# Kernel tuning notes

Hardware: AMD Instinct MI355X
Metric: run time of the kernel (lower is better)

Reference implementation:

```python
import jax, jax.numpy as jnp
import numpy as np

N = 50000          # num nodes
E = 800000         # num edges
DIN = 128          # in_channels
C = 64             # out_channels per head
H = 2              # heads
ED = 32            # edge_dim


def setup_inputs() -> dict:
    key = jax.random.key(0)
    ks = jax.random.split(key, 12)
    s = 1.0 / np.sqrt(DIN)
    se = 1.0 / np.sqrt(ED)
    return {
        "x": jax.random.normal(ks[0], (N, DIN), dtype=jnp.float32),
        "edge_index": jax.random.randint(ks[1], (2, E), 0, N, dtype=jnp.int32),
        "edge_attr": jax.random.normal(ks[2], (E, ED), dtype=jnp.float32),
        "Wq": jax.random.uniform(ks[3], (DIN, H * C), jnp.float32, -s, s),
        "bq": jax.random.uniform(ks[4], (H * C,), jnp.float32, -s, s),
        "Wk": jax.random.uniform(ks[5], (DIN, H * C), jnp.float32, -s, s),
        "bk": jax.random.uniform(ks[6], (H * C,), jnp.float32, -s, s),
        "Wv": jax.random.uniform(ks[7], (DIN, H * C), jnp.float32, -s, s),
        "bv": jax.random.uniform(ks[8], (H * C,), jnp.float32, -s, s),
        "We": jax.random.uniform(ks[9], (ED, H * C), jnp.float32, -se, se),
        "Wskip": jax.random.uniform(ks[10], (DIN, H * C), jnp.float32, -s, s),
        "bskip": jax.random.uniform(ks[11], (H * C,), jnp.float32, -s, s),
    }


def reference(x, edge_index, edge_attr, Wq, bq, Wk, bk, Wv, bv, We, Wskip, bskip):
    src, dst = edge_index[0], edge_index[1]
    # node-level projections [N, H, C]
    q = (x @ Wq + bq).reshape(N, H, C)
    k = (x @ Wk + bk).reshape(N, H, C)
    v = (x @ Wv + bv).reshape(N, H, C)
    e = (edge_attr @ We).reshape(E, H, C)  # lin_edge, no bias

    # per-edge gather
    q_e = q[dst]              # [E, H, C]
    k_e = k[src] + e          # key gets edge features
    alpha = jnp.einsum("ehc,ehc->eh", q_e, k_e) / jnp.sqrt(jnp.float32(C))

    # segment softmax over incoming edges of each dst node
    m = jax.ops.segment_max(alpha, dst, num_segments=N)       # [N, H]
    alpha = jnp.exp(alpha - m[dst])
    denom = jax.ops.segment_sum(alpha, dst, num_segments=N)   # [N, H]
    alpha = alpha / (denom[dst] + 1e-16)

    # weighted aggregation of values (value also gets edge features)
    msg = (v[src] + e) * alpha[..., None]                     # [E, H, C]
    out = jax.ops.segment_sum(msg, dst, num_segments=N)       # [N, H, C]
    out = out.reshape(N, H * C)

    # root weight skip connection (concat=True, beta=False)
    return out + x @ Wskip + bskip
```

## Files before the change

kernel.cpp:

```cpp
#include <hip/hip_runtime.h>
#include <cstdint>

#define NN 50000
#define EE 800000
#define DINC 128
#define HC 128
#define EDC 32
#define CAP 56
#define TILES 1563
#define GEMM_BLKS 6252
#define SCAT_BLKS 3125
#define NB_SCAN 196

typedef __attribute__((ext_vector_type(8))) short short8;
typedef __attribute__((ext_vector_type(4))) float floatx4;

__device__ __forceinline__ unsigned int pk2(float a, float b){
  unsigned int ua = __float_as_uint(a), ub = __float_as_uint(b);
  ua = (ua + 0x7FFFu + ((ua >> 16) & 1u)) >> 16;
  ub = (ub + 0x7FFFu + ((ub >> 16) & 1u)) & 0xFFFF0000u;
  return ua | ub;
}
__device__ __forceinline__ float bflo(unsigned int p){ return __uint_as_float(p << 16); }
__device__ __forceinline__ float bfhi(unsigned int p){ return __uint_as_float(p & 0xFFFF0000u); }

__global__ __launch_bounds__(256) void k_prew(
    const float* __restrict__ Wq, const float* __restrict__ Wk,
    const float* __restrict__ Wv, const float* __restrict__ Wsk,
    unsigned int* __restrict__ Wp)
{
  int idx = blockIdx.x*256 + threadIdx.x;
  int mat = idx >> 13;
  int r   = idx & 8191;
  int kp  = r >> 7;
  int n   = r & 127;
  const float* W = (mat==0)?Wq:(mat==1)?Wk:(mat==2)?Wv:Wsk;
  Wp[(mat<<13) + n*64 + kp] = pk2(W[(2*kp)*HC + n], W[(2*kp+1)*HC + n]);
}

__global__ __launch_bounds__(256) void k_fused(
    const float* __restrict__ x, const unsigned int* __restrict__ Wp,
    const float* __restrict__ bq, const float* __restrict__ bk,
    const float* __restrict__ bv, const float* __restrict__ bsk,
    const int* __restrict__ ei,
    unsigned int* __restrict__ qbf, unsigned int* __restrict__ kvb,
    float* __restrict__ out, int* __restrict__ cnt, int* __restrict__ eidl,
    const int do_scatter)
{
  __shared__ unsigned int smem[32*132];

  if (do_scatter && blockIdx.x >= GEMM_BLKS){
    int e = (blockIdx.x - GEMM_BLKS)*256 + threadIdx.x;
    if (e < EE){
      int d = ei[EE + e];
      int pos = atomicAdd(cnt + d, 1);
      if (pos < CAP) eidl[d*CAP + pos] = e;
    }
    return;
  }

  unsigned int* sx = smem;
  float* facc = (float*)smem;

  const int tid = threadIdx.x;
  const int mat = blockIdx.x & 3;
  const int bm  = (blockIdx.x >> 2) * 32;
  const float* bi = (mat==0)?bq:(mat==1)?bk:(mat==2)?bv:bsk;
  const unsigned int* wp = Wp + (mat<<13);

  for (int idx = tid; idx < 32*32; idx += 256){
    int row = idx >> 5, kq = idx & 31;
    int gr = bm + row;
    unsigned int p0 = 0u, p1 = 0u;
    if (gr < NN){
      float4 v = *(const float4*)(x + (size_t)gr*DINC + 4*kq);
      p0 = pk2(v.x, v.y); p1 = pk2(v.z, v.w);
    }
    sx[row*68 + 2*kq]     = p0;
    sx[row*68 + 2*kq + 1] = p1;
  }
  __syncthreads();

  const int l = tid & 63, wid = tid >> 6;
  const int lm = l & 15, ks = l >> 4;
  const int n0 = wid * 32;

  floatx4 acc[2][2];
  #pragma unroll
  for (int mt=0;mt<2;mt++)
    #pragma unroll
    for (int nt=0;nt<2;nt++) acc[mt][nt] = (floatx4){0.f,0.f,0.f,0.f};

  #pragma unroll
  for (int kb = 0; kb < 4; ++kb){
    short8 a0 = *(const short8*)(sx + lm*68        + kb*16 + ks*4);
    short8 a1 = *(const short8*)(sx + (16+lm)*68   + kb*16 + ks*4);
    short8 b0 = *(const short8*)(wp + (n0+lm)*64    + kb*16 + ks*4);
    short8 b1 = *(const short8*)(wp + (n0+16+lm)*64 + kb*16 + ks*4);
    acc[0][0] = __builtin_amdgcn_mfma_f32_16x16x32_bf16(a0, b0, acc[0][0], 0, 0, 0);
    acc[0][1] = __builtin_amdgcn_mfma_f32_16x16x32_bf16(a0, b1, acc[0][1], 0, 0, 0);
    acc[1][0] = __builtin_amdgcn_mfma_f32_16x16x32_bf16(a1, b0, acc[1][0], 0, 0, 0);
    acc[1][1] = __builtin_amdgcn_mfma_f32_16x16x32_bf16(a1, b1, acc[1][1], 0, 0, 0);
  }
  __syncthreads();

  #pragma unroll
  for (int mt=0;mt<2;mt++)
    #pragma unroll
    for (int nt=0;nt<2;nt++)
      #pragma unroll
      for (int r=0;r<4;r++){
        int row = mt*16 + ks*4 + r;
        int col = n0 + nt*16 + lm;
        facc[row*132 + col] = acc[mt][nt][r];
      }
  __syncthreads();

  for (int idx = tid; idx < 32*64; idx += 256){
    int row = idx >> 6, cp = idx & 63;
    int gr = bm + row;
    if (gr >= NN) continue;
    float2 vv = *(const float2*)(facc + row*132 + 2*cp);
    float2 bb = *(const float2*)(bi + 2*cp);
    float v0 = vv.x + bb.x, v1 = vv.y + bb.y;
    if (mat == 0)      qbf[gr*64 + cp] = pk2(v0, v1);
    else if (mat == 1) kvb[(size_t)gr*128 + cp]      = pk2(v0, v1);
    else if (mat == 2) kvb[(size_t)gr*128 + 64 + cp] = pk2(v0, v1);
    else *(float2*)(out + (size_t)gr*HC + 2*cp) = make_float2(v0, v1);
  }
}

__global__ __launch_bounds__(256) void k_count(const int* __restrict__ ei,
    int* __restrict__ cnt)
{
  int e = blockIdx.x*256 + threadIdx.x;
  if (e < EE) atomicAdd(cnt + ei[EE + e], 1);
}
__global__ __launch_bounds__(256) void k_blksum(const int* __restrict__ cnt,
    int* __restrict__ bsum)
{
  __shared__ int s[256];
  int t = threadIdx.x, i = blockIdx.x*256 + t;
  s[t] = (i < NN) ? cnt[i] : 0;
  __syncthreads();
  for (int d = 128; d > 0; d >>= 1){
    if (t < d) s[t] += s[t + d];
    __syncthreads();
  }
  if (t == 0) bsum[blockIdx.x] = s[0];
}
__global__ __launch_bounds__(256) void k_bscan(const int* __restrict__ bsum,
    int* __restrict__ bpre)
{
  __shared__ int s[256];
  int t = threadIdx.x;
  int v = (t < NB_SCAN) ? bsum[t] : 0;
  s[t] = v;
  __syncthreads();
  for (int d = 1; d < 256; d <<= 1){
    int u = (t >= d) ? s[t - d] : 0;
    __syncthreads();
    s[t] += u;
    __syncthreads();
  }
  if (t < NB_SCAN) bpre[t] = s[t] - v;
}
__global__ __launch_bounds__(256) void k_scan3(const int* __restrict__ cnt,
    const int* __restrict__ bpre, int* __restrict__ off, int* __restrict__ woff)
{
  __shared__ int s[256];
  int t = threadIdx.x, i = blockIdx.x*256 + t;
  int v = (i < NN) ? cnt[i] : 0;
  s[t] = v;
  __syncthreads();
  for (int d = 1; d < 256; d <<= 1){
    int u = (t >= d) ? s[t - d] : 0;
    __syncthreads();
    s[t] += u;
    __syncthreads();
  }
  if (i < NN){
    int o = bpre[blockIdx.x] + s[t] - v;
    off[i] = o; woff[i] = o;
  }
}
__global__ __launch_bounds__(256) void k_scatter(const int* __restrict__ ei,
    int* __restrict__ woff, int* __restrict__ eidl)
{
  int e = blockIdx.x*256 + threadIdx.x;
  if (e < EE){
    int d = ei[EE + e];
    int pos = atomicAdd(woff + d, 1);
    eidl[pos] = e;
  }
}

__global__ __launch_bounds__(256) void k_agg(
    const float* __restrict__ eattr, const float* __restrict__ We,
    const unsigned int* __restrict__ qbf, const unsigned int* __restrict__ kvb,
    const int* __restrict__ ei,
    const int* __restrict__ cnt, const int* __restrict__ off,
    const int* __restrict__ eidl, const int fixed,
    float* __restrict__ out)
{
  __shared__ float sWeT[128*33];
  const int tid = threadIdx.x;
  for (int idx = tid; idx < EDC*HC; idx += 256){
    int jj = idx >> 7, col = idx & 127;
    sWeT[col*33 + jj] = We[idx];
  }
  __syncthreads();

  const int wid = tid >> 6, l = tid & 63;
  const int node = blockIdx.x*4 + wid;
  const int h = l >> 5, j = l & 31;

  int deg = cnt[node]; if (deg > CAP) deg = CAP;
  const size_t beg = fixed ? (size_t)node*CAP : (size_t)off[node];
  int eidL = 0, srcL = 0;
  if (deg > 0){
    eidL = eidl[beg + ((l < deg) ? l : 0)];
    srcL = ei[eidL];
  }

  unsigned int qp = qbf[node*64 + l];
  float q0 = bflo(qp), q1 = bfhi(qp);
  float Pl = 0.f;
  {
    const unsigned int* qrow = qbf + node*64 + h*32;
    const float* wt = sWeT + (h*64)*33 + j;
    #pragma unroll 8
    for (int cc = 0; cc < 32; ++cc){
      unsigned int up = qrow[cc];
      Pl += bflo(up)*wt[(2*cc)*33] + bfhi(up)*wt[(2*cc+1)*33];
    }
  }

  float acc0=0.f, acc1=0.f, wea=0.f, den=0.f;
  if (deg > 0){
    float eav[4]; unsigned int kk[4], vv[4];
    #pragma unroll
    for (int t = 0; t < 4; ++t){
      int it  = (t < deg) ? t : 0;
      int eid = __shfl(eidL, it, 64);
      int src = __shfl(srcL, it, 64);
      eav[t] = eattr[(size_t)eid*EDC + j];
      kk[t]  = kvb[(size_t)src*128 + l];
      vv[t]  = kvb[(size_t)src*128 + 64 + l];
    }
    for (int i = 0; i < deg; i += 4){
      float eavn[4]; unsigned int kkn[4], vvn[4];
      const int inext = i + 4;
      if (inext < deg){
        #pragma unroll
        for (int t = 0; t < 4; ++t){
          int it  = (inext + t < deg) ? inext + t : inext;
          int eid = __shfl(eidL, it, 64);
          int src = __shfl(srcL, it, 64);
          eavn[t] = eattr[(size_t)eid*EDC + j];
          kkn[t]  = kvb[(size_t)src*128 + l];
          vvn[t]  = kvb[(size_t)src*128 + 64 + l];
        }
      }
      float p[4];
      #pragma unroll
      for (int t = 0; t < 4; ++t)
        p[t] = q0*bflo(kk[t]) + q1*bfhi(kk[t]) + Pl*eav[t];
      #pragma unroll
      for (int s = 1; s < 32; s <<= 1){
        #pragma unroll
        for (int t = 0; t < 4; ++t) p[t] += __shfl_xor(p[t], s, 32);
      }
      const int nb = deg - i;
      #pragma unroll
      for (int t = 0; t < 4; ++t){
        float a = __expf(p[t] * 0.125f);
        if (t > 0) a = (t < nb) ? a : 0.f;
        den  += a;
        acc0 += a*bflo(vv[t]);
        acc1 += a*bfhi(vv[t]);
        wea  += a*eav[t];
      }
      #pragma unroll
      for (int t = 0; t < 4; ++t){ eav[t] = eavn[t]; kk[t] = kkn[t]; vv[t] = vvn[t]; }
    }
  }

  float rden = 1.0f/(den + 1e-16f);
  float e0 = 0.f, e1 = 0.f;
  const float* w0 = sWeT + (2*l)*33;
  const float* w1 = sWeT + (2*l+1)*33;
  #pragma unroll 8
  for (int jj = 0; jj < 32; ++jj){
    float w = __shfl(wea, h*32 + jj, 64);
    e0 += w*w0[jj]; e1 += w*w1[jj];
  }
  float2 sk = *(const float2*)(out + (size_t)node*HC + 2*l);
  float2 o;
  o.x = sk.x + (acc0 + e0)*rden;
  o.y = sk.y + (acc1 + e1)*rden;
  *(float2*)(out + (size_t)node*HC + 2*l) = o;
}

extern "C" void kernel_launch(void* const* d_in, const int* in_sizes, int n_in,
                              void* d_out, int out_size, void* d_ws, size_t ws_size,
                              hipStream_t stream)
{
  const float* x   = (const float*)d_in[0];
  const int*   ei  = (const int*)d_in[1];
  const float* ea  = (const float*)d_in[2];
  const float* Wq  = (const float*)d_in[3];
  const float* bq  = (const float*)d_in[4];
  const float* Wk  = (const float*)d_in[5];
  const float* bk  = (const float*)d_in[6];
  const float* Wv  = (const float*)d_in[7];
  const float* bv  = (const float*)d_in[8];
  const float* We  = (const float*)d_in[9];
  const float* Wsk = (const float*)d_in[10];
  const float* bsk = (const float*)d_in[11];
  float* out = (float*)d_out;

  char* ws = (char*)d_ws;
  unsigned int* qbf = (unsigned int*)(ws);
  unsigned int* kvb = (unsigned int*)(ws + 12800000);
  int* cnt = (int*)(ws + 38400000);

  hipMemsetAsync(cnt, 0, NN*sizeof(int), stream);

  if (ws_size >= 50000000ull){
    int* eidl = (int*)(ws + 38600000);
    unsigned int* Wp = (unsigned int*)(ws + 49800064);
    k_prew<<<128, 256, 0, stream>>>(Wq, Wk, Wv, Wsk, Wp);
    k_fused<<<GEMM_BLKS + SCAT_BLKS, 256, 0, stream>>>(
        x, Wp, bq, bk, bv, bsk, ei, qbf, kvb, out, cnt, eidl, 1);
    k_agg<<<12500, 256, 0, stream>>>(ea, We, qbf, kvb, ei,
                                     cnt, (const int*)nullptr, eidl, 1, out);
  } else {
    int* off  = (int*)(ws + 38600000);
    int* woff = (int*)(ws + 38800000);
    int* bsum = (int*)(ws + 39000000);
    int* bpre = (int*)(ws + 39001024);
    int* eidl = (int*)(ws + 39002048);
    unsigned int* Wp = (unsigned int*)(ws + 42202112);
    k_prew<<<128, 256, 0, stream>>>(Wq, Wk, Wv, Wsk, Wp);
    k_fused<<<GEMM_BLKS, 256, 0, stream>>>(
        x, Wp, bq, bk, bv, bsk, ei, qbf, kvb, out, cnt, nullptr, 0);
    k_count  <<<SCAT_BLKS, 256, 0, stream>>>(ei, cnt);
    k_blksum <<<NB_SCAN, 256, 0, stream>>>(cnt, bsum);
    k_bscan  <<<1, 256, 0, stream>>>(bsum, bpre);
    k_scan3  <<<NB_SCAN, 256, 0, stream>>>(cnt, bpre, off, woff);
    k_scatter<<<SCAT_BLKS, 256, 0, stream>>>(ei, woff, eidl);
    k_agg<<<12500, 256, 0, stream>>>(ea, We, qbf, kvb, ei,
                                     cnt, off, eidl, 0, out);
  }
}
```

Baseline: 411.2 us.

## Deepen aggregation prefetch to two stages and transpose-reduce edge dot products

The edge loop now prefetches two groups of four edges ahead instead of one, to hide more gather latency. Each lane loads edges in an XOR-permuted order so that four per-edge dot products can be reduced with a transposed butterfly. This replaces 20 shuffles per group with 8 shuffles plus 3 to redistribute the softmax weights, and computes one exp per lane instead of four. The extra in-flight buffers raise register pressure and may lower occupancy.

```diff
diff --git a/kernel.cpp b/kernel.cpp
--- a/kernel.cpp
+++ b/kernel.cpp
@@ -213,7 +213,8 @@
 
   const int wid = tid >> 6, l = tid & 63;
   const int node = blockIdx.x*4 + wid;
-  const int h = l >> 5, j = l & 31;
+  const int h = l >> 5, ch = l & 31;
+  const int t0 = l & 3;
 
   int deg = cnt[node]; if (deg > CAP) deg = CAP;
   const size_t beg = fixed ? (size_t)node*CAP : (size_t)off[node];
@@ -228,7 +229,7 @@
   float Pl = 0.f;
   {
     const unsigned int* qrow = qbf + node*64 + h*32;
-    const float* wt = sWeT + (h*64)*33 + j;
+    const float* wt = sWeT + (h*64)*33 + ch;
     #pragma unroll 8
     for (int cc = 0; cc < 32; ++cc){
       unsigned int up = qrow[cc];
@@ -236,55 +237,65 @@
     }
   }
 
+#define GATHER(base, EA, KK, VV)                        \
+  {                                                     \
+    _Pragma("unroll")                                   \
+    for (int jx = 0; jx < 4; ++jx){                     \
+      int s = (base) + (t0 ^ jx);                       \
+      int it = (s < deg) ? s : 0;                       \
+      int eid = __shfl(eidL, it, 64);                   \
+      int src = __shfl(srcL, it, 64);                   \
+      EA[jx] = eattr[(size_t)eid*EDC + ch];             \
+      KK[jx] = kvb[(size_t)src*128 + l];                \
+      VV[jx] = kvb[(size_t)src*128 + 64 + l];           \
+    }                                                   \
+  }
+
   float acc0=0.f, acc1=0.f, wea=0.f, den=0.f;
   if (deg > 0){
-    float eav[4]; unsigned int kk[4], vv[4];
-    #pragma unroll
-    for (int t = 0; t < 4; ++t){
-      int it  = (t < deg) ? t : 0;
-      int eid = __shfl(eidL, it, 64);
-      int src = __shfl(srcL, it, 64);
-      eav[t] = eattr[(size_t)eid*EDC + j];
-      kk[t]  = kvb[(size_t)src*128 + l];
-      vv[t]  = kvb[(size_t)src*128 + 64 + l];
+    float eav[4], eav1[4];
+    unsigned int kk[4], vv[4], kk1[4], vv1[4];
+    GATHER(0, eav, kk, vv);
+    GATHER(4, eav1, kk1, vv1);
+
+    for (int i = 0; i < deg; i += 4){
+      float eavn[4] = {0.f,0.f,0.f,0.f};
+      unsigned int kkn[4] = {0u,0u,0u,0u}, vvn[4] = {0u,0u,0u,0u};
+      if (i + 8 < deg){ GATHER(i+8, eavn, kkn, vvn); }
+
+      float p0 = q0*bflo(kk[0]) + q1*bfhi(kk[0]) + Pl*eav[0];
+      float p1 = q0*bflo(kk[1]) + q1*bfhi(kk[1]) + Pl*eav[1];
+      float p2 = q0*bflo(kk[2]) + q1*bfhi(kk[2]) + Pl*eav[2];
+      float p3 = q0*bflo(kk[3]) + q1*bfhi(kk[3]) + Pl*eav[3];
+
+      float q01 = p0 + __shfl_xor(p1, 1, 32);
+      float q23 = p2 + __shfl_xor(p3, 1, 32);
+      float r   = q01 + __shfl_xor(q23, 2, 32);
+      r += __shfl_xor(r, 4, 32);
+      r += __shfl_xor(r, 8, 32);
+      r += __shfl_xor(r, 16, 32);
+
+      float a = __expf(r * 0.125f);
+      const int nb = deg - i;
+      if (t0 >= nb) a = 0.f;
+
+      float b1 = __shfl_xor(a, 1, 32);
+      float b2 = __shfl_xor(a, 2, 32);
+      float b3 = __shfl_xor(b1, 2, 32);
+
+      den  += (a + b1) + (b2 + b3);
+      acc0 += a*bflo(vv[0]) + b1*bflo(vv[1]) + b2*bflo(vv[2]) + b3*bflo(vv[3]);
+      acc1 += a*bfhi(vv[0]) + b1*bfhi(vv[1]) + b2*bfhi(vv[2]) + b3*bfhi(vv[3]);
+      wea  += a*eav[0] + b1*eav[1] + b2*eav[2] + b3*eav[3];
+
+      #pragma unroll
+      for (int jx = 0; jx < 4; ++jx){
+        eav[jx] = eav1[jx]; kk[jx] = kk1[jx]; vv[jx] = vv1[jx];
+        eav1[jx] = eavn[jx]; kk1[jx] = kkn[jx]; vv1[jx] = vvn[jx];
+      }
     }
-    for (int i = 0; i < deg; i += 4){
-      float eavn[4]; unsigned int kkn[4], vvn[4];
-      const int inext = i + 4;
-      if (inext < deg){
-        #pragma unroll
-        for (int t = 0; t < 4; ++t){
-          int it  = (inext + t < deg) ? inext + t : inext;
-          int eid = __shfl(eidL, it, 64);
-          int src = __shfl(srcL, it, 64);
-          eavn[t] = eattr[(size_t)eid*EDC + j];
-          kkn[t]  = kvb[(size_t)src*128 + l];
-          vvn[t]  = kvb[(size_t)src*128 + 64 + l];
-        }
-      }
-      float p[4];
-      #pragma unroll
-      for (int t = 0; t < 4; ++t)
-        p[t] = q0*bflo(kk[t]) + q1*bfhi(kk[t]) + Pl*eav[t];
-      #pragma unroll
-      for (int s = 1; s < 32; s <<= 1){
-        #pragma unroll
-        for (int t = 0; t < 4; ++t) p[t] += __shfl_xor(p[t], s, 32);
-      }
-      const int nb = deg - i;
-      #pragma unroll
-      for (int t = 0; t < 4; ++t){
-        float a = __expf(p[t] * 0.125f);
-        if (t > 0) a = (t < nb) ? a : 0.f;
-        den  += a;
-        acc0 += a*bflo(vv[t]);
-        acc1 += a*bfhi(vv[t]);
-        wea  += a*eav[t];
-      }
-      #pragma unroll
-      for (int t = 0; t < 4; ++t){ eav[t] = eavn[t]; kk[t] = kkn[t]; vv[t] = vvn[t]; }
-    }
-  }
+  }
+#undef GATHER
 
   float rden = 1.0f/(den + 1e-16f);
   float e0 = 0.f, e1 = 0.f;
```

New measurement: 439.1 us. +6.8%, slower.

## Compute all four projections per x tile and tighten aggregation gathers

Applied to the files above, without the earlier changes.

The projection kernel now loads and converts each 32-row x tile once and loops over all four weight matrices inside the block, cutting the GEMM grid from four blocks per tile to one. Separate shared buffers let the tile persist while the accumulator staging is reused. The aggregation kernel precomputes 32-bit byte offsets for its edge and key/value gathers, vectorizes the q-row loads, and replaces the per-element shuffle broadcast of the weighted edge sums with a shared-memory exchange. This trades GEMM parallelism and extra shared memory for less redundant x traffic and fewer address and shuffle instructions.

```diff
diff --git a/kernel.cpp b/kernel.cpp
--- a/kernel.cpp
+++ b/kernel.cpp
@@ -8,7 +8,6 @@
 #define EDC 32
 #define CAP 56
 #define TILES 1563
-#define GEMM_BLKS 6252
 #define SCAT_BLKS 3125
 #define NB_SCAN 196
 
@@ -47,10 +46,11 @@
     float* __restrict__ out, int* __restrict__ cnt, int* __restrict__ eidl,
     const int do_scatter)
 {
-  __shared__ unsigned int smem[32*132];
-
-  if (do_scatter && blockIdx.x >= GEMM_BLKS){
-    int e = (blockIdx.x - GEMM_BLKS)*256 + threadIdx.x;
+  __shared__ unsigned int sx[32*68];
+  __shared__ float facc[32*132];
+
+  if (do_scatter && blockIdx.x >= TILES){
+    int e = (blockIdx.x - TILES)*256 + threadIdx.x;
     if (e < EE){
       int d = ei[EE + e];
       int pos = atomicAdd(cnt + d, 1);
@@ -59,14 +59,8 @@
     return;
   }
 
-  unsigned int* sx = smem;
-  float* facc = (float*)smem;
-
   const int tid = threadIdx.x;
-  const int mat = blockIdx.x & 3;
-  const int bm  = (blockIdx.x >> 2) * 32;
-  const float* bi = (mat==0)?bq:(mat==1)?bk:(mat==2)?bv:bsk;
-  const unsigned int* wp = Wp + (mat<<13);
+  const int bm  = blockIdx.x * 32;
 
   for (int idx = tid; idx < 32*32; idx += 256){
     int row = idx >> 5, kq = idx & 31;
@@ -85,48 +79,54 @@
   const int lm = l & 15, ks = l >> 4;
   const int n0 = wid * 32;
 
-  floatx4 acc[2][2];
   #pragma unroll
-  for (int mt=0;mt<2;mt++)
+  for (int mat = 0; mat < 4; ++mat){
+    const unsigned int* wp = Wp + (mat<<13);
+    const float* bi = (mat==0)?bq:(mat==1)?bk:(mat==2)?bv:bsk;
+
+    floatx4 acc[2][2];
     #pragma unroll
-    for (int nt=0;nt<2;nt++) acc[mt][nt] = (floatx4){0.f,0.f,0.f,0.f};
-
-  #pragma unroll
-  for (int kb = 0; kb < 4; ++kb){
-    short8 a0 = *(const short8*)(sx + lm*68        + kb*16 + ks*4);
-    short8 a1 = *(const short8*)(sx + (16+lm)*68   + kb*16 + ks*4);
-    short8 b0 = *(const short8*)(wp + (n0+lm)*64    + kb*16 + ks*4);
-    short8 b1 = *(const short8*)(wp + (n0+16+lm)*64 + kb*16 + ks*4);
-    acc[0][0] = __builtin_amdgcn_mfma_f32_16x16x32_bf16(a0, b0, acc[0][0], 0, 0, 0);
-    acc[0][1] = __builtin_amdgcn_mfma_f32_16x16x32_bf16(a0, b1, acc[0][1], 0, 0, 0);
-    acc[1][0] = __builtin_amdgcn_mfma_f32_16x16x32_bf16(a1, b0, acc[1][0], 0, 0, 0);
-    acc[1][1] = __builtin_amdgcn_mfma_f32_16x16x32_bf16(a1, b1, acc[1][1], 0, 0, 0);
-  }
-  __syncthreads();
-
-  #pragma unroll
-  for (int mt=0;mt<2;mt++)
+    for (int mt=0;mt<2;mt++)
+      #pragma unroll
+      for (int nt=0;nt<2;nt++) acc[mt][nt] = (floatx4){0.f,0.f,0.f,0.f};
+
     #pragma unroll
-    for (int nt=0;nt<2;nt++)
-      #pragma unroll
-      for (int r=0;r<4;r++){
-        int row = mt*16 + ks*4 + r;
-        int col = n0 + nt*16 + lm;
-        facc[row*132 + col] = acc[mt][nt][r];
-      }
-  __syncthreads();
-
-  for (int idx = tid; idx < 32*64; idx += 256){
-    int row = idx >> 6, cp = idx & 63;
-    int gr = bm + row;
-    if (gr >= NN) continue;
-    float2 vv = *(const float2*)(facc + row*132 + 2*cp);
-    float2 bb = *(const float2*)(bi + 2*cp);
-    float v0 = vv.x + bb.x, v1 = vv.y + bb.y;
-    if (mat == 0)      qbf[gr*64 + cp] = pk2(v0, v1);
-    else if (mat == 1) kvb[(size_t)gr*128 + cp]      = pk2(v0, v1);
-    else if (mat == 2) kvb[(size_t)gr*128 + 64 + cp] = pk2(v0, v1);
-    else *(float2*)(out + (size_t)gr*HC + 2*cp) = make_float2(v0, v1);
+    for (int kb = 0; kb < 4; ++kb){
+      short8 a0 = *(const short8*)(sx + lm*68        + kb*16 + ks*4);
+      short8 a1 = *(const short8*)(sx + (16+lm)*68   + kb*16 + ks*4);
+      short8 b0 = *(const short8*)(wp + (n0+lm)*64    + kb*16 + ks*4);
+      short8 b1 = *(const short8*)(wp + (n0+16+lm)*64 + kb*16 + ks*4);
+      acc[0][0] = __builtin_amdgcn_mfma_f32_16x16x32_bf16(a0, b0, acc[0][0], 0, 0, 0);
+      acc[0][1] = __builtin_amdgcn_mfma_f32_16x16x32_bf16(a0, b1, acc[0][1], 0, 0, 0);
+      acc[1][0] = __builtin_amdgcn_mfma_f32_16x16x32_bf16(a1, b0, acc[1][0], 0, 0, 0);
+      acc[1][1] = __builtin_amdgcn_mfma_f32_16x16x32_bf16(a1, b1, acc[1][1], 0, 0, 0);
+    }
+    __syncthreads();
+
+    #pragma unroll
+    for (int mt=0;mt<2;mt++)
+      #pragma unroll
+      for (int nt=0;nt<2;nt++)
+        #pragma unroll
+        for (int r=0;r<4;r++){
+          int row = mt*16 + ks*4 + r;
+          int col = n0 + nt*16 + lm;
+          facc[row*132 + col] = acc[mt][nt][r];
+        }
+    __syncthreads();
+
+    for (int idx = tid; idx < 32*64; idx += 256){
+      int row = idx >> 6, cp = idx & 63;
+      int gr = bm + row;
+      if (gr >= NN) continue;
+      float2 vv = *(const float2*)(facc + row*132 + 2*cp);
+      float2 bb = *(const float2*)(bi + 2*cp);
+      float v0 = vv.x + bb.x, v1 = vv.y + bb.y;
+      if (mat == 0)      qbf[gr*64 + cp] = pk2(v0, v1);
+      else if (mat == 1) kvb[(size_t)gr*128 + cp]      = pk2(v0, v1);
+      else if (mat == 2) kvb[(size_t)gr*128 + 64 + cp] = pk2(v0, v1);
+      else *(float2*)(out + (size_t)gr*HC + 2*cp) = make_float2(v0, v1);
+    }
   }
 }
 
@@ -204,6 +204,7 @@
     float* __restrict__ out)
 {
   __shared__ float sWeT[128*33];
+  __shared__ float sWea[256];
   const int tid = threadIdx.x;
   for (int idx = tid; idx < EDC*HC; idx += 256){
     int jj = idx >> 7, col = idx & 127;
@@ -222,45 +223,54 @@
     eidL = eidl[beg + ((l < deg) ? l : 0)];
     srcL = ei[eidL];
   }
+  const unsigned int eaOff = (unsigned int)eidL * (EDC*4);
+  const unsigned int kOff  = (unsigned int)srcL * 512u;
+  const unsigned int jB = (unsigned int)j * 4u;
+  const unsigned int lB = (unsigned int)l * 4u;
+  const char* eac = (const char*)eattr;
+  const char* kvc = (const char*)kvb;
 
   unsigned int qp = qbf[node*64 + l];
   float q0 = bflo(qp), q1 = bfhi(qp);
   float Pl = 0.f;
   {
-    const unsigned int* qrow = qbf + node*64 + h*32;
+    const uint4* qrow4 = (const uint4*)(qbf + node*64 + h*32);
     const float* wt = sWeT + (h*64)*33 + j;
-    #pragma unroll 8
-    for (int cc = 0; cc < 32; ++cc){
-      unsigned int up = qrow[cc];
-      Pl += bflo(up)*wt[(2*cc)*33] + bfhi(up)*wt[(2*cc+1)*33];
-    }
+    #pragma unroll
+    for (int c4 = 0; c4 < 8; ++c4){
+      uint4 u = qrow4[c4];
+      int b = 8*c4;
+      Pl += bflo(u.x)*wt[(b+0)*33] + bfhi(u.x)*wt[(b+1)*33];
+      Pl += bflo(u.y)*wt[(b+2)*33] + bfhi(u.y)*wt[(b+3)*33];
+      Pl += bflo(u.z)*wt[(b+4)*33] + bfhi(u.z)*wt[(b+5)*33];
+      Pl += bflo(u.w)*wt[(b+6)*33] + bfhi(u.w)*wt[(b+7)*33];
+    }
+  }
+
+#define GATHER(base, EA, KK, VV)                                 \
+  {                                                              \
+    _Pragma("unroll")                                            \
+    for (int t = 0; t < 4; ++t){                                 \
+      int s = (base) + t;                                        \
+      int it = (s < deg) ? s : 0;                                \
+      unsigned int eo = (unsigned int)__shfl((int)eaOff, it, 64) + jB; \
+      unsigned int ko = (unsigned int)__shfl((int)kOff,  it, 64) + lB; \
+      EA[t] = *(const float*)(eac + eo);                         \
+      KK[t] = *(const unsigned int*)(kvc + ko);                  \
+      VV[t] = *(const unsigned int*)(kvc + ko + 256);            \
+    }                                                            \
   }
 
   float acc0=0.f, acc1=0.f, wea=0.f, den=0.f;
   if (deg > 0){
     float eav[4]; unsigned int kk[4], vv[4];
-    #pragma unroll
-    for (int t = 0; t < 4; ++t){
-      int it  = (t < deg) ? t : 0;
-      int eid = __shfl(eidL, it, 64);
-      int src = __shfl(srcL, it, 64);
-      eav[t] = eattr[(size_t)eid*EDC + j];
-      kk[t]  = kvb[(size_t)src*128 + l];
-      vv[t]  = kvb[(size_t)src*128 + 64 + l];
-    }
+    GATHER(0, eav, kk, vv);
+
     for (int i = 0; i < deg; i += 4){
       float eavn[4]; unsigned int kkn[4], vvn[4];
       const int inext = i + 4;
       if (inext < deg){
-        #pragma unroll
-        for (int t = 0; t < 4; ++t){
-          int it  = (inext + t < deg) ? inext + t : inext;
-          int eid = __shfl(eidL, it, 64);
-          int src = __shfl(srcL, it, 64);
-          eavn[t] = eattr[(size_t)eid*EDC + j];
-          kkn[t]  = kvb[(size_t)src*128 + l];
-          vvn[t]  = kvb[(size_t)src*128 + 64 + l];
-        }
+        GATHER(inext, eavn, kkn, vvn);
       }
       float p[4];
       #pragma unroll
@@ -285,15 +295,22 @@
       for (int t = 0; t < 4; ++t){ eav[t] = eavn[t]; kk[t] = kkn[t]; vv[t] = vvn[t]; }
     }
   }
-
+#undef GATHER
+
+  sWea[tid] = wea;
+  __syncthreads();
   float rden = 1.0f/(den + 1e-16f);
   float e0 = 0.f, e1 = 0.f;
   const float* w0 = sWeT + (2*l)*33;
   const float* w1 = sWeT + (2*l+1)*33;
-  #pragma unroll 8
-  for (int jj = 0; jj < 32; ++jj){
-    float w = __shfl(wea, h*32 + jj, 64);
-    e0 += w*w0[jj]; e1 += w*w1[jj];
+  const float* wv = sWea + wid*64 + h*32;
+  #pragma unroll
+  for (int jj = 0; jj < 32; jj += 4){
+    float4 w4 = *(const float4*)(wv + jj);
+    e0 += w4.x*w0[jj]; e1 += w4.x*w1[jj];
+    e0 += w4.y*w0[jj+1]; e1 += w4.y*w1[jj+1];
+    e0 += w4.z*w0[jj+2]; e1 += w4.z*w1[jj+2];
+    e0 += w4.w*w0[jj+3]; e1 += w4.w*w1[jj+3];
   }
   float2 sk = *(const float2*)(out + (size_t)node*HC + 2*l);
   float2 o;
@@ -331,7 +348,7 @@
     int* eidl = (int*)(ws + 38600000);
     unsigned int* Wp = (unsigned int*)(ws + 49800064);
     k_prew<<<128, 256, 0, stream>>>(Wq, Wk, Wv, Wsk, Wp);
-    k_fused<<<GEMM_BLKS + SCAT_BLKS, 256, 0, stream>>>(
+    k_fused<<<TILES + SCAT_BLKS, 256, 0, stream>>>(
         x, Wp, bq, bk, bv, bsk, ei, qbf, kvb, out, cnt, eidl, 1);
     k_agg<<<12500, 256, 0, stream>>>(ea, We, qbf, kvb, ei,
                                      cnt, (const int*)nullptr, eidl, 1, out);
@@ -343,7 +360,7 @@
     int* eidl = (int*)(ws + 39002048);
     unsigned int* Wp = (unsigned int*)(ws + 42202112);
     k_prew<<<128, 256, 0, stream>>>(Wq, Wk, Wv, Wsk, Wp);
-    k_fused<<<GEMM_BLKS, 256, 0, stream>>>(
+    k_fused<<<TILES, 256, 0, stream>>>(
         x, Wp, bq, bk, bv, bsk, ei, qbf, kvb, out, cnt, nullptr, 0);
     k_count  <<<SCAT_BLKS, 256, 0, stream>>>(ei, cnt);
     k_blksum <<<NB_SCAN, 256, 0, stream>>>(cnt, bsum);
```

After: 411.5 us. About the same (+0.1%).
